# Performance work log

Measured on AMD Instinct MI355X. Metric: run time of the kernel, lower is better.

Reference implementation:

```python
import jax, jax.numpy as jnp
import numpy as np

B, A, C = 1, 196416, 90
H = W = 1024
SCORE_THRESHOLD = 0.05
MAX_DETECTIONS = 100
# RetinaNet-style BBoxTransform normalization (mean=0, std=[0.1,0.1,0.2,0.2])
STD = (0.1, 0.1, 0.2, 0.2)


def setup_inputs() -> dict:
    key = jax.random.key(0)
    k1, k2, k3, k4, k5, k6, k7 = jax.random.split(key, 7)
    x = jax.random.normal(k1, (B, 3, H, W), dtype=jnp.float32)
    regression = jax.random.normal(k2, (B, A, 4), dtype=jnp.float32) * 0.1
    classification = jax.random.normal(k3, (B, A, C), dtype=jnp.float32)
    # valid anchor boxes (x1, y1, x2, y2)
    cx = jax.random.uniform(k4, (B, A), minval=0.0, maxval=float(W))
    cy = jax.random.uniform(k5, (B, A), minval=0.0, maxval=float(H))
    aw = jax.random.uniform(k6, (B, A), minval=16.0, maxval=256.0)
    ah = jax.random.uniform(k7, (B, A), minval=16.0, maxval=256.0)
    anchors = jnp.stack([cx - 0.5 * aw, cy - 0.5 * ah, cx + 0.5 * aw, cy + 0.5 * ah], axis=2).astype(jnp.float32)
    return {"x": x, "regression": regression, "classification": classification, "anchors": anchors}


def _decode_clip(anchors, regression, img_h, img_w):
    # BBoxTransform: deltas (dx, dy, dw, dh) scaled by std, applied to anchor center/size
    wa = anchors[..., 2] - anchors[..., 0]
    ha = anchors[..., 3] - anchors[..., 1]
    cxa = anchors[..., 0] + 0.5 * wa
    cya = anchors[..., 1] + 0.5 * ha
    dx = regression[..., 0] * STD[0]
    dy = regression[..., 1] * STD[1]
    dw = regression[..., 2] * STD[2]
    dh = regression[..., 3] * STD[3]
    cx = cxa + dx * wa
    cy = cya + dy * ha
    w = jnp.exp(dw) * wa
    h = jnp.exp(dh) * ha
    # ClipBoxes: x1,y1 clamped at 0; x2,y2 clamped at image width/height
    x1 = jnp.maximum(cx - 0.5 * w, 0.0)
    y1 = jnp.maximum(cy - 0.5 * h, 0.0)
    x2 = jnp.minimum(cx + 0.5 * w, float(img_w))
    y2 = jnp.minimum(cy + 0.5 * h, float(img_h))
    return jnp.stack([x1, y1, x2, y2], axis=2)  # [B, A, 4]


def reference(x, regression, classification, anchors):
    img_h, img_w = x.shape[2], x.shape[3]
    boxes = _decode_clip(anchors, regression, img_h, img_w)  # [1, A, 4]
    probs = jax.nn.sigmoid(classification)                    # [1, A, C]
    scores = jnp.max(probs, axis=2)                           # [1, A]
    classes = jnp.argmax(probs, axis=2)                       # [1, A]
    valid_scores = jnp.where(scores > SCORE_THRESHOLD, scores, 0.0)
    vb = boxes[0]            # [A, 4]
    vc = classes[0]          # [A]
    vs = valid_scores[0]     # [A]
    k = min(MAX_DETECTIONS, vs.shape[0])
    _, top_idx = jax.lax.top_k(vs, k)
    final_boxes = vb[top_idx]
    final_scores = vs[top_idx]
    final_classes = vc[top_idx]
    return (final_boxes, final_scores, final_classes)
```

## Files before the change

kernel.cpp:

```cpp
#include <hip/hip_runtime.h>
#include <cmath>

#define A_CNT 196416
#define C_CNT 90
#define PAIRS (A_CNT / 2)
#define WITERS 12276
#define TOPK 100u
#define CAPB 2048
#define NB_RED 1536
#define NB_GAT 192

#define OFF_HIST1 785664u
#define OFF_CTRL  789760u
#define OFF_CANDA 789824u
#define OFF_CANDB 790336u

#define AGENT_LD(p)    __hip_atomic_load((p), __ATOMIC_RELAXED, __HIP_MEMORY_SCOPE_AGENT)
#define AGENT_ST(p, v) __hip_atomic_store((p), (v), __ATOMIC_RELAXED, __HIP_MEMORY_SCOPE_AGENT)

__global__ __launch_bounds__(256, 4) void k_reduce(const float* __restrict__ cls,
                                                   unsigned* __restrict__ keys,
                                                   unsigned* __restrict__ hist1,
                                                   unsigned* __restrict__ ctrl) {
    __shared__ unsigned lhist[576];
    __shared__ unsigned sdata[256];
    __shared__ unsigned sbin[2];
    __shared__ int sflag;
    const int t = threadIdx.x;
    for (int j = t; j < 576; j += 256) lhist[j] = 0u;
    __syncthreads();

    const int lane = t & 63;
    const int g = lane >> 3, s = lane & 7;
    const int wid = blockIdx.x * 4 + (t >> 6);
    const int nw = NB_RED * 4;
    const float4* __restrict__ cls4 = (const float4*)cls;

    for (int w = wid; w < WITERS; w += nw) {
        const int p = w * 8 + g;
        const float4* __restrict__ r4 = cls4 + (size_t)p * 45;
        float m0 = -INFINITY, m1 = -INFINITY;
#pragma unroll
        for (int i = 0; i < 6; ++i) {
            const int j = s + 8 * i;
            if (j < 45) {
                float4 v = r4[j];
                float a01 = fmaxf(v.x, v.y), a23 = fmaxf(v.z, v.w);
                float all = fmaxf(a01, a23);
                if (j < 22)      m0 = fmaxf(m0, all);
                else if (j > 22) m1 = fmaxf(m1, all);
                else { m0 = fmaxf(m0, a01); m1 = fmaxf(m1, a23); }
            }
        }
#pragma unroll
        for (int d = 1; d < 8; d <<= 1) {
            m0 = fmaxf(m0, __shfl_xor(m0, d));
            m1 = fmaxf(m1, __shfl_xor(m1, d));
        }
        if (s == 0) {
            float p0 = 1.0f / (1.0f + expf(-m0));
            float p1 = 1.0f / (1.0f + expf(-m1));
            unsigned k0 = (p0 > 0.05f) ? __float_as_uint(p0) : 0u;
            unsigned k1 = (p1 > 0.05f) ? __float_as_uint(p1) : 0u;
            *(uint2*)(keys + 2 * p) = make_uint2(k0, k1);
            unsigned h0 = k0 ? (min(k0 >> 16, 0x3F80u) - 0x3D4Bu) : 0u;
            unsigned h1 = k1 ? (min(k1 >> 16, 0x3F80u) - 0x3D4Bu) : 0u;
            atomicAdd(&lhist[h0], 1u);
            atomicAdd(&lhist[h1], 1u);
        }
    }
    __syncthreads();
    for (int j = t; j < 576; j += 256) {
        unsigned c = lhist[j];
        if (c) atomicAdd(&hist1[j], c);
    }
    __syncthreads();
    if (t == 0) sflag = (atomicAdd(&ctrl[8], 1u) == NB_RED - 1u) ? 1 : 0;
    __syncthreads();
    if (!sflag) return;

    const unsigned target = TOPK;
    unsigned ssum = 0;
#pragma unroll
    for (int j = 0; j < 4; ++j) ssum += AGENT_LD(&hist1[t * 4 + j]);
    sdata[t] = ssum;
    for (int d = 1; d < 256; d <<= 1) {
        __syncthreads();
        unsigned add = (t + d < 256) ? sdata[t + d] : 0u;
        __syncthreads();
        sdata[t] += add;
    }
    __syncthreads();
    {
        unsigned mysuf  = sdata[t];
        unsigned nxtsuf = (t < 255) ? sdata[t + 1] : 0u;
        if (nxtsuf < target && mysuf >= target) { sbin[0] = (unsigned)t; sbin[1] = nxtsuf; }
    }
    __syncthreads();
    const unsigned chunkB = sbin[0];
    const unsigned gAbove = sbin[1];
    unsigned v = (t < 4) ? AGENT_LD(&hist1[chunkB * 4 + t]) : 0u;
    sdata[t] = v;
    for (int d = 1; d < 256; d <<= 1) {
        __syncthreads();
        unsigned add = (t + d < 256) ? sdata[t + d] : 0u;
        __syncthreads();
        sdata[t] += add;
    }
    __syncthreads();
    {
        unsigned mysuf  = sdata[t] + gAbove;
        unsigned nxtsuf = ((t < 255) ? sdata[t + 1] : 0u) + gAbove;
        if (nxtsuf < target && mysuf >= target) {
            unsigned bin = chunkB * 4 + (unsigned)t;
            ctrl[0] = bin ? (bin + 0x3D4Bu) : 0u;
            ctrl[1] = nxtsuf;
        }
    }
}

__global__ __launch_bounds__(256) void k_gather(const float* __restrict__ cls,
                                                const float* __restrict__ reg,
                                                const float* __restrict__ anc,
                                                const unsigned* __restrict__ keys,
                                                unsigned* __restrict__ ctrl,
                                                unsigned* __restrict__ candA,
                                                unsigned* __restrict__ candB,
                                                float* __restrict__ out) {
    __shared__ unsigned sAi[128], sAk[128];
    __shared__ unsigned sBi[CAPB], sBk[CAPB];
    __shared__ unsigned sel[TOPK];
    __shared__ int sflag;
    const int t = threadIdx.x;

    const unsigned binB = ctrl[0];
    const int i4 = blockIdx.x * 256 + t;
    if (i4 < A_CNT / 4) {
        uint4 k = ((const uint4*)keys)[i4];
        const unsigned base = (unsigned)(4 * i4);
#pragma unroll
        for (int j = 0; j < 4; ++j) {
            unsigned kk = (j == 0) ? k.x : (j == 1) ? k.y : (j == 2) ? k.z : k.w;
            unsigned t16 = kk >> 16;
            if (t16 > binB) {
                unsigned q = atomicAdd(&ctrl[5], 1u);
                if (q < 128u) AGENT_ST(&candA[q], base + j);
            } else if (t16 == binB) {
                unsigned q = atomicAdd(&ctrl[6], 1u);
                if (q < (unsigned)CAPB) AGENT_ST(&candB[q], base + j);
            }
        }
    }
    __syncthreads();
    if (t == 0) sflag = (atomicAdd(&ctrl[9], 1u) == (unsigned)NB_GAT - 1u) ? 1 : 0;
    __syncthreads();
    if (!sflag) return;

    const unsigned nA = min(AGENT_LD(&ctrl[5]), 128u);
    const unsigned nB = min(AGENT_LD(&ctrl[6]), (unsigned)CAPB);
    const unsigned need = TOPK - nA;

    if (t < (int)nA) { unsigned i = AGENT_LD(&candA[t]); sAi[t] = i; sAk[t] = keys[i]; }
    for (unsigned e = (unsigned)t; e < nB; e += 256u) {
        unsigned i = AGENT_LD(&candB[e]); sBi[e] = i; sBk[e] = keys[i];
    }
    __syncthreads();

    if (t < (int)nA) {
        unsigned mi = sAi[t], mk = sAk[t], r = 0;
        for (unsigned j = 0; j < nA; ++j) {
            unsigned ok = sAk[j];
            if (ok > mk || (ok == mk && sAi[j] < mi)) r++;
        }
        sel[r] = mi;
    }
    for (unsigned e = (unsigned)t; e < nB; e += 256u) {
        unsigned mi = sBi[e], mk = sBk[e], r = 0;
        for (unsigned j = 0; j < nB; ++j) {
            unsigned ok = sBk[j];
            if (ok > mk || (ok == mk && sBi[j] < mi)) r++;
        }
        if (r < need) sel[nA + r] = mi;
    }
    __syncthreads();

    if (t < (int)TOPK) {
        const unsigned a = sel[t];
        const float2* row = (const float2*)(cls + (size_t)a * C_CNT);
        float bv = -INFINITY; int bi = 0;
#pragma unroll 5
        for (int c = 0; c < 45; ++c) {
            float2 v = row[c];
            if (v.x > bv) { bv = v.x; bi = 2 * c; }
            if (v.y > bv) { bv = v.y; bi = 2 * c + 1; }
        }
        float score = __uint_as_float(keys[a]);
        float x1a = anc[a * 4 + 0], y1a = anc[a * 4 + 1];
        float x2a = anc[a * 4 + 2], y2a = anc[a * 4 + 3];
        float wa = x2a - x1a, ha = y2a - y1a;
        float cxa = x1a + 0.5f * wa, cya = y1a + 0.5f * ha;
        float dx = reg[a * 4 + 0] * 0.1f, dy = reg[a * 4 + 1] * 0.1f;
        float dw = reg[a * 4 + 2] * 0.2f, dh = reg[a * 4 + 3] * 0.2f;
        float cx = cxa + dx * wa, cy = cya + dy * ha;
        float w = expf(dw) * wa, h = expf(dh) * ha;
        out[t * 4 + 0] = fmaxf(cx - 0.5f * w, 0.0f);
        out[t * 4 + 1] = fmaxf(cy - 0.5f * h, 0.0f);
        out[t * 4 + 2] = fminf(cx + 0.5f * w, 1024.0f);
        out[t * 4 + 3] = fminf(cy + 0.5f * h, 1024.0f);
        out[400 + t] = score;
        out[500 + t] = (float)bi;
    }
}

extern "C" void kernel_launch(void* const* d_in, const int* in_sizes, int n_in,
                              void* d_out, int out_size, void* d_ws, size_t ws_size,
                              hipStream_t stream) {
    const float* reg = (const float*)d_in[1];
    const float* cls = (const float*)d_in[2];
    const float* anc = (const float*)d_in[3];
    float* out = (float*)d_out;
    char* ws = (char*)d_ws;
    unsigned* keys  = (unsigned*)ws;
    unsigned* hist1 = (unsigned*)(ws + OFF_HIST1);
    unsigned* ctrl  = (unsigned*)(ws + OFF_CTRL);
    unsigned* candA = (unsigned*)(ws + OFF_CANDA);
    unsigned* candB = (unsigned*)(ws + OFF_CANDB);

    hipMemsetAsync(hist1, 0, 4096 + 64, stream);
    k_reduce<<<NB_RED, 256, 0, stream>>>(cls, keys, hist1, ctrl);
    k_gather<<<NB_GAT, 256, 0, stream>>>(cls, reg, anc, keys, ctrl, candA, candB, out);
}
```

Baseline: 153.1 us.

## Fuse reduce and gather into one cooperative kernel keeping keys in LDS

Merges the two kernels into a single cooperative launch of 1024 blocks that uses grid-wide syncs between the histogram, threshold, and candidate phases. Per-anchor keys stay in shared memory instead of round-tripping through a global keys buffer, and every block computes the threshold bin redundantly rather than relying on a last-block pattern. Candidate keys are stored next to their indices. This removes a kernel launch and the global key writes and re-reads, at the cost of two grid barriers and the residency constraint of a cooperative launch. Larger shared memory per block (about 20KB) may limit occupancy.

```diff
diff --git a/kernel.cpp b/kernel.cpp
--- a/kernel.cpp
+++ b/kernel.cpp
@@ -1,5 +1,8 @@
 #include <hip/hip_runtime.h>
+#include <hip/hip_cooperative_groups.h>
 #include <cmath>
+
+namespace cg = cooperative_groups;
 
 #define A_CNT 196416
 #define C_CNT 90
@@ -7,66 +10,83 @@
 #define WITERS 12276
 #define TOPK 100u
 #define CAPB 2048
-#define NB_RED 1536
-#define NB_GAT 192
-
-#define OFF_HIST1 785664u
-#define OFF_CTRL  789760u
-#define OFF_CANDA 789824u
-#define OFF_CANDB 790336u
+#define NBLK 1024
+#define NWAVE (NBLK * 4)
+
+#define OFF_CTRL 4096u
+#define OFF_CAI  4160u
+#define OFF_CAK  4672u
+#define OFF_CBI  5184u
+#define OFF_CBK  13376u
 
 #define AGENT_LD(p)    __hip_atomic_load((p), __ATOMIC_RELAXED, __HIP_MEMORY_SCOPE_AGENT)
 #define AGENT_ST(p, v) __hip_atomic_store((p), (v), __ATOMIC_RELAXED, __HIP_MEMORY_SCOPE_AGENT)
 
-__global__ __launch_bounds__(256, 4) void k_reduce(const float* __restrict__ cls,
-                                                   unsigned* __restrict__ keys,
-                                                   unsigned* __restrict__ hist1,
-                                                   unsigned* __restrict__ ctrl) {
+__global__ __launch_bounds__(256, 4) void k_all(const float* __restrict__ cls,
+                                                const float* __restrict__ reg,
+                                                const float* __restrict__ anc,
+                                                unsigned* __restrict__ hist1,
+                                                unsigned* __restrict__ ctrl,
+                                                unsigned* __restrict__ cAi,
+                                                unsigned* __restrict__ cAk,
+                                                unsigned* __restrict__ cBi,
+                                                unsigned* __restrict__ cBk,
+                                                float* __restrict__ out) {
     __shared__ unsigned lhist[576];
-    __shared__ unsigned sdata[256];
-    __shared__ unsigned sbin[2];
-    __shared__ int sflag;
+    __shared__ unsigned skey[192], sanchor[192];
+    __shared__ unsigned sdata[256], sres[2];
+    __shared__ unsigned sAi[128], sAk[128];
+    __shared__ unsigned sBi[CAPB], sBk[CAPB];
+    __shared__ unsigned selI[TOPK], selK[TOPK];
+
     const int t = threadIdx.x;
     for (int j = t; j < 576; j += 256) lhist[j] = 0u;
+    if (t < 192) sanchor[t] = 0xFFFFFFFFu;
     __syncthreads();
 
     const int lane = t & 63;
     const int g = lane >> 3, s = lane & 7;
-    const int wid = blockIdx.x * 4 + (t >> 6);
-    const int nw = NB_RED * 4;
+    const int wl = t >> 6;
+    const int W = blockIdx.x * 4 + wl;
     const float4* __restrict__ cls4 = (const float4*)cls;
 
-    for (int w = wid; w < WITERS; w += nw) {
-        const int p = w * 8 + g;
-        const float4* __restrict__ r4 = cls4 + (size_t)p * 45;
-        float m0 = -INFINITY, m1 = -INFINITY;
-#pragma unroll
-        for (int i = 0; i < 6; ++i) {
-            const int j = s + 8 * i;
-            if (j < 45) {
-                float4 v = r4[j];
-                float a01 = fmaxf(v.x, v.y), a23 = fmaxf(v.z, v.w);
-                float all = fmaxf(a01, a23);
-                if (j < 22)      m0 = fmaxf(m0, all);
-                else if (j > 22) m1 = fmaxf(m1, all);
-                else { m0 = fmaxf(m0, a01); m1 = fmaxf(m1, a23); }
-            }
-        }
-#pragma unroll
-        for (int d = 1; d < 8; d <<= 1) {
-            m0 = fmaxf(m0, __shfl_xor(m0, d));
-            m1 = fmaxf(m1, __shfl_xor(m1, d));
-        }
-        if (s == 0) {
-            float p0 = 1.0f / (1.0f + expf(-m0));
-            float p1 = 1.0f / (1.0f + expf(-m1));
-            unsigned k0 = (p0 > 0.05f) ? __float_as_uint(p0) : 0u;
-            unsigned k1 = (p1 > 0.05f) ? __float_as_uint(p1) : 0u;
-            *(uint2*)(keys + 2 * p) = make_uint2(k0, k1);
-            unsigned h0 = k0 ? (min(k0 >> 16, 0x3F80u) - 0x3D4Bu) : 0u;
-            unsigned h1 = k1 ? (min(k1 >> 16, 0x3F80u) - 0x3D4Bu) : 0u;
-            atomicAdd(&lhist[h0], 1u);
-            atomicAdd(&lhist[h1], 1u);
+#pragma unroll
+    for (int it = 0; it < 3; ++it) {
+        const int w = W + it * NWAVE;
+        if (w < WITERS) {
+            const int p = w * 8 + g;
+            const float4* __restrict__ r4 = cls4 + (size_t)p * 45;
+            float m0 = -INFINITY, m1 = -INFINITY;
+#pragma unroll
+            for (int i = 0; i < 6; ++i) {
+                const int j = s + 8 * i;
+                if (j < 45) {
+                    float4 v = r4[j];
+                    float a01 = fmaxf(v.x, v.y), a23 = fmaxf(v.z, v.w);
+                    float all = fmaxf(a01, a23);
+                    if (j < 22)      m0 = fmaxf(m0, all);
+                    else if (j > 22) m1 = fmaxf(m1, all);
+                    else { m0 = fmaxf(m0, a01); m1 = fmaxf(m1, a23); }
+                }
+            }
+#pragma unroll
+            for (int d = 1; d < 8; d <<= 1) {
+                m0 = fmaxf(m0, __shfl_xor(m0, d));
+                m1 = fmaxf(m1, __shfl_xor(m1, d));
+            }
+            if (s == 0) {
+                float p0 = 1.0f / (1.0f + expf(-m0));
+                float p1 = 1.0f / (1.0f + expf(-m1));
+                unsigned k0 = (p0 > 0.05f) ? __float_as_uint(p0) : 0u;
+                unsigned k1 = (p1 > 0.05f) ? __float_as_uint(p1) : 0u;
+                const int sb = wl * 48 + it * 16 + g * 2;
+                skey[sb] = k0;     skey[sb + 1] = k1;
+                sanchor[sb] = 2u * p; sanchor[sb + 1] = 2u * p + 1u;
+                unsigned h0 = k0 ? (min(k0 >> 16, 0x3F80u) - 0x3D4Bu) : 0u;
+                unsigned h1 = k1 ? (min(k1 >> 16, 0x3F80u) - 0x3D4Bu) : 0u;
+                atomicAdd(&lhist[h0], 1u);
+                atomicAdd(&lhist[h1], 1u);
+            }
         }
     }
     __syncthreads();
@@ -74,95 +94,74 @@
         unsigned c = lhist[j];
         if (c) atomicAdd(&hist1[j], c);
     }
-    __syncthreads();
-    if (t == 0) sflag = (atomicAdd(&ctrl[8], 1u) == NB_RED - 1u) ? 1 : 0;
-    __syncthreads();
-    if (!sflag) return;
-
-    const unsigned target = TOPK;
-    unsigned ssum = 0;
-#pragma unroll
-    for (int j = 0; j < 4; ++j) ssum += AGENT_LD(&hist1[t * 4 + j]);
-    sdata[t] = ssum;
-    for (int d = 1; d < 256; d <<= 1) {
-        __syncthreads();
-        unsigned add = (t + d < 256) ? sdata[t + d] : 0u;
-        __syncthreads();
-        sdata[t] += add;
-    }
-    __syncthreads();
+
+    cg::this_grid().sync();
+
     {
-        unsigned mysuf  = sdata[t];
-        unsigned nxtsuf = (t < 255) ? sdata[t + 1] : 0u;
-        if (nxtsuf < target && mysuf >= target) { sbin[0] = (unsigned)t; sbin[1] = nxtsuf; }
-    }
-    __syncthreads();
-    const unsigned chunkB = sbin[0];
-    const unsigned gAbove = sbin[1];
-    unsigned v = (t < 4) ? AGENT_LD(&hist1[chunkB * 4 + t]) : 0u;
-    sdata[t] = v;
-    for (int d = 1; d < 256; d <<= 1) {
-        __syncthreads();
-        unsigned add = (t + d < 256) ? sdata[t + d] : 0u;
-        __syncthreads();
-        sdata[t] += add;
-    }
-    __syncthreads();
-    {
-        unsigned mysuf  = sdata[t] + gAbove;
-        unsigned nxtsuf = ((t < 255) ? sdata[t + 1] : 0u) + gAbove;
-        if (nxtsuf < target && mysuf >= target) {
-            unsigned bin = chunkB * 4 + (unsigned)t;
-            ctrl[0] = bin ? (bin + 0x3D4Bu) : 0u;
-            ctrl[1] = nxtsuf;
-        }
-    }
-}
-
-__global__ __launch_bounds__(256) void k_gather(const float* __restrict__ cls,
-                                                const float* __restrict__ reg,
-                                                const float* __restrict__ anc,
-                                                const unsigned* __restrict__ keys,
-                                                unsigned* __restrict__ ctrl,
-                                                unsigned* __restrict__ candA,
-                                                unsigned* __restrict__ candB,
-                                                float* __restrict__ out) {
-    __shared__ unsigned sAi[128], sAk[128];
-    __shared__ unsigned sBi[CAPB], sBk[CAPB];
-    __shared__ unsigned sel[TOPK];
-    __shared__ int sflag;
-    const int t = threadIdx.x;
-
-    const unsigned binB = ctrl[0];
-    const int i4 = blockIdx.x * 256 + t;
-    if (i4 < A_CNT / 4) {
-        uint4 k = ((const uint4*)keys)[i4];
-        const unsigned base = (unsigned)(4 * i4);
-#pragma unroll
-        for (int j = 0; j < 4; ++j) {
-            unsigned kk = (j == 0) ? k.x : (j == 1) ? k.y : (j == 2) ? k.z : k.w;
-            unsigned t16 = kk >> 16;
+        unsigned ssum = 0;
+#pragma unroll
+        for (int j = 0; j < 4; ++j) ssum += AGENT_LD(&hist1[t * 4 + j]);
+        sdata[t] = ssum;
+        for (int d = 1; d < 256; d <<= 1) {
+            __syncthreads();
+            unsigned add = (t + d < 256) ? sdata[t + d] : 0u;
+            __syncthreads();
+            sdata[t] += add;
+        }
+        __syncthreads();
+        {
+            unsigned mysuf  = sdata[t];
+            unsigned nxtsuf = (t < 255) ? sdata[t + 1] : 0u;
+            if (nxtsuf < TOPK && mysuf >= TOPK) { sres[0] = (unsigned)t; sres[1] = nxtsuf; }
+        }
+        __syncthreads();
+        const unsigned chunkB = sres[0];
+        const unsigned gAbove = sres[1];
+        unsigned v = (t < 4) ? AGENT_LD(&hist1[chunkB * 4 + t]) : 0u;
+        sdata[t] = v;
+        for (int d = 1; d < 256; d <<= 1) {
+            __syncthreads();
+            unsigned add = (t + d < 256) ? sdata[t + d] : 0u;
+            __syncthreads();
+            sdata[t] += add;
+        }
+        __syncthreads();
+        {
+            unsigned mysuf  = sdata[t] + gAbove;
+            unsigned nxtsuf = ((t < 255) ? sdata[t + 1] : 0u) + gAbove;
+            if (nxtsuf < TOPK && mysuf >= TOPK) {
+                unsigned bin = chunkB * 4 + (unsigned)t;
+                sres[0] = bin ? (bin + 0x3D4Bu) : 0u;
+            }
+        }
+        __syncthreads();
+    }
+    const unsigned binB = sres[0];
+
+    if (t < 192) {
+        unsigned a = sanchor[t];
+        if (a != 0xFFFFFFFFu) {
+            unsigned kk = skey[t], t16 = kk >> 16;
             if (t16 > binB) {
                 unsigned q = atomicAdd(&ctrl[5], 1u);
-                if (q < 128u) AGENT_ST(&candA[q], base + j);
+                if (q < 128u) { AGENT_ST(&cAi[q], a); AGENT_ST(&cAk[q], kk); }
             } else if (t16 == binB) {
                 unsigned q = atomicAdd(&ctrl[6], 1u);
-                if (q < (unsigned)CAPB) AGENT_ST(&candB[q], base + j);
-            }
-        }
-    }
-    __syncthreads();
-    if (t == 0) sflag = (atomicAdd(&ctrl[9], 1u) == (unsigned)NB_GAT - 1u) ? 1 : 0;
-    __syncthreads();
-    if (!sflag) return;
-
+                if (q < (unsigned)CAPB) { AGENT_ST(&cBi[q], a); AGENT_ST(&cBk[q], kk); }
+            }
+        }
+    }
+
+    cg::this_grid().sync();
+
+    if (blockIdx.x != 0) return;
     const unsigned nA = min(AGENT_LD(&ctrl[5]), 128u);
     const unsigned nB = min(AGENT_LD(&ctrl[6]), (unsigned)CAPB);
-    const unsigned need = TOPK - nA;
-
-    if (t < (int)nA) { unsigned i = AGENT_LD(&candA[t]); sAi[t] = i; sAk[t] = keys[i]; }
+    const unsigned need = (nA < TOPK) ? (TOPK - nA) : 0u;
+
+    if (t < (int)nA) { sAi[t] = AGENT_LD(&cAi[t]); sAk[t] = AGENT_LD(&cAk[t]); }
     for (unsigned e = (unsigned)t; e < nB; e += 256u) {
-        unsigned i = AGENT_LD(&candB[e]); sBi[e] = i; sBk[e] = keys[i];
+        sBi[e] = AGENT_LD(&cBi[e]); sBk[e] = AGENT_LD(&cBk[e]);
     }
     __syncthreads();
 
@@ -172,7 +171,7 @@
             unsigned ok = sAk[j];
             if (ok > mk || (ok == mk && sAi[j] < mi)) r++;
         }
-        sel[r] = mi;
+        selI[r] = mi; selK[r] = mk;
     }
     for (unsigned e = (unsigned)t; e < nB; e += 256u) {
         unsigned mi = sBi[e], mk = sBk[e], r = 0;
@@ -180,12 +179,12 @@
             unsigned ok = sBk[j];
             if (ok > mk || (ok == mk && sBi[j] < mi)) r++;
         }
-        if (r < need) sel[nA + r] = mi;
+        if (r < need) { selI[nA + r] = mi; selK[nA + r] = mk; }
     }
     __syncthreads();
 
     if (t < (int)TOPK) {
-        const unsigned a = sel[t];
+        const unsigned a = selI[t];
         const float2* row = (const float2*)(cls + (size_t)a * C_CNT);
         float bv = -INFINITY; int bi = 0;
 #pragma unroll 5
@@ -194,7 +193,7 @@
             if (v.x > bv) { bv = v.x; bi = 2 * c; }
             if (v.y > bv) { bv = v.y; bi = 2 * c + 1; }
         }
-        float score = __uint_as_float(keys[a]);
+        float score = __uint_as_float(selK[t]);
         float x1a = anc[a * 4 + 0], y1a = anc[a * 4 + 1];
         float x2a = anc[a * 4 + 2], y2a = anc[a * 4 + 3];
         float wa = x2a - x1a, ha = y2a - y1a;
@@ -220,13 +219,16 @@
     const float* anc = (const float*)d_in[3];
     float* out = (float*)d_out;
     char* ws = (char*)d_ws;
-    unsigned* keys  = (unsigned*)ws;
-    unsigned* hist1 = (unsigned*)(ws + OFF_HIST1);
+    unsigned* hist1 = (unsigned*)ws;
     unsigned* ctrl  = (unsigned*)(ws + OFF_CTRL);
-    unsigned* candA = (unsigned*)(ws + OFF_CANDA);
-    unsigned* candB = (unsigned*)(ws + OFF_CANDB);
+    unsigned* cAi   = (unsigned*)(ws + OFF_CAI);
+    unsigned* cAk   = (unsigned*)(ws + OFF_CAK);
+    unsigned* cBi   = (unsigned*)(ws + OFF_CBI);
+    unsigned* cBk   = (unsigned*)(ws + OFF_CBK);
 
     hipMemsetAsync(hist1, 0, 4096 + 64, stream);
-    k_reduce<<<NB_RED, 256, 0, stream>>>(cls, keys, hist1, ctrl);
-    k_gather<<<NB_GAT, 256, 0, stream>>>(cls, reg, anc, keys, ctrl, candA, candB, out);
+
+    void* args[] = {(void*)&cls, (void*)&reg, (void*)&anc, (void*)&hist1, (void*)&ctrl,
+                    (void*)&cAi, (void*)&cAk, (void*)&cBi, (void*)&cBk, (void*)&out};
+    hipLaunchCooperativeKernel((void*)k_all, dim3(NBLK), dim3(256), args, 0, stream);
 }
```

Measured after the change: 329.5 us. 2.15x slower.
